# Performance work log

Measured on AMD Instinct MI355X. Metric: run time of the kernel, lower is better.

The kernel has to match this reference:

```python
import jax, jax.numpy as jnp
import numpy as np

N_EMB = 1024
N_HEAD = 16
HD = N_EMB // N_HEAD
ROPE_BASE = 10000.0


def _rope_cos_sin(seq_len, dim, dtype):
    inv_freq = 1.0 / (ROPE_BASE ** (jnp.arange(0, dim, 2, dtype=jnp.float32) / dim))
    t = jnp.arange(seq_len, dtype=jnp.float32)
    freqs = jnp.outer(t, inv_freq)              # [S, dim/2]
    emb = jnp.concatenate([freqs, freqs], -1)    # [S, dim]
    return jnp.cos(emb).astype(dtype), jnp.sin(emb).astype(dtype)


def _rotate_half(x):
    x1, x2 = jnp.split(x, 2, axis=-1)
    return jnp.concatenate([-x2, x1], axis=-1)


def _apply_rope(x):
    # x: [B, H, L, hd]; rotary over sequence axis (-2)
    cos, sin = _rope_cos_sin(x.shape[-2], x.shape[-1], x.dtype)
    return x * cos + _rotate_half(x) * sin


def setup_inputs() -> dict:
    key = jax.random.key(0)
    ks = jax.random.split(key, 8)
    B, T, S = 2, 2048, 2048
    std = 0.02
    return {
        "x": jax.random.normal(ks[0], (B, T, N_EMB), jnp.float32),
        "memory": jax.random.normal(ks[1], (B, S, N_EMB), jnp.float32),
        "q_w": jax.random.normal(ks[2], (N_EMB, N_EMB), jnp.float32) * std,
        "q_b": jnp.zeros((N_EMB,), jnp.float32),
        "kv_w": jax.random.normal(ks[3], (N_EMB, 2 * N_EMB), jnp.float32) * std,
        "kv_b": jnp.zeros((2 * N_EMB,), jnp.float32),
        "proj_w": jax.random.normal(ks[4], (N_EMB, N_EMB), jnp.float32) * std,
        "proj_b": jnp.zeros((N_EMB,), jnp.float32),
    }


def reference(x, memory, q_w, q_b, kv_w, kv_b, proj_w, proj_b):
    B, S, C = memory.shape
    T = x.shape[1]
    kv = memory @ kv_w + kv_b                      # [B,S,2C]
    K, V = jnp.split(kv, 2, axis=-1)
    Q = x @ q_w + q_b                              # [B,T,C]

    def heads(t, L):
        return t.reshape(B, L, N_HEAD, HD).transpose(0, 2, 1, 3)

    Q, K, V = heads(Q, T), heads(K, S), heads(V, S)
    Q = jax.nn.elu(Q) + 1.0                        # positive feature map
    K = jax.nn.elu(K) + 1.0
    Q_rot = _apply_rope(Q)
    K_rot = _apply_rope(K)
    # denom row-sum: sum_s Q.K_s == Q . (sum_s K_s) -- identical math, no SxT matrix
    denom = jnp.einsum('bhtd,bhd->bht', Q, K.sum(axis=2))[..., None]  # [B,H,T,1]
    att = jnp.einsum('bhtd,bhsd->bhts', Q_rot, K_rot) / denom          # [B,H,T,S]
    y = jnp.einsum('bhts,bhsd->bhtd', att, V)                          # [B,H,T,hd]
    y = y.transpose(0, 2, 1, 3).reshape(B, T, C)
    return y @ proj_w + proj_b
```

## Files before the change

### kernel.cpp

```cpp
#include <hip/hip_runtime.h>
#include <cstddef>
#include <cstdint>

#define B_SZ  2
#define T_SEQ 2048
#define S_SEQ 2048
#define C_EMB 1024
#define NH    16
#define HD    64
#define KDIM  1024

typedef __attribute__((ext_vector_type(8))) short bf16x8;
typedef __attribute__((ext_vector_type(4))) float f32x4;

#define OFF_XH    ((size_t)0)
#define OFF_XL    ((size_t)2097152)
#define OFF_MEMH  ((size_t)4194304)
#define OFF_MEML  ((size_t)6291456)
#define OFF_QWH   ((size_t)8388608)
#define OFF_QWL   ((size_t)8912896)
#define OFF_KVWH  ((size_t)9437184)
#define OFF_KVWL  ((size_t)10485760)
#define OFF_PWH   ((size_t)11534336)
#define OFF_PWL   ((size_t)12058624)
#define OFF_KSUM  ((size_t)12582912)
#define OFF_MT    ((size_t)12584960)
#define OFF_TAB   ((size_t)12716032)
#define OFF_YH    ((size_t)12847104)
#define OFF_YL    ((size_t)14944256)
#define WS_FLOATS ((size_t)17041408)

__device__ __forceinline__ float elu1(float v) {
    return v > 0.0f ? v + 1.0f : __expf(v);
}
__device__ __forceinline__ unsigned short bf16_rne(float x) {
    union { float f; unsigned int u; } v; v.f = x;
    unsigned int u = v.u;
    return (unsigned short)((u + 0x7FFFu + ((u >> 16) & 1u)) >> 16);
}
__device__ __forceinline__ float bf16_to_f(unsigned short h) {
    union { unsigned int u; float f; } v; v.u = ((unsigned int)h) << 16;
    return v.f;
}

#define PREP_BLOCKS 13064

__device__ __forceinline__ void split4_body(
    const float4* __restrict__ in, ushort4* __restrict__ hi,
    ushort4* __restrict__ lo, int i)
{
    float4 v = in[i];
    ushort4 h, l;
    h.x = bf16_rne(v.x); l.x = bf16_rne(v.x - bf16_to_f(h.x));
    h.y = bf16_rne(v.y); l.y = bf16_rne(v.y - bf16_to_f(h.y));
    h.z = bf16_rne(v.z); l.z = bf16_rne(v.z - bf16_to_f(h.z));
    h.w = bf16_rne(v.w); l.w = bf16_rne(v.w - bf16_to_f(h.w));
    hi[i] = h; lo[i] = l;
}

__device__ __forceinline__ void transpose_body(
    const float* __restrict__ W, unsigned short* __restrict__ Wth,
    unsigned short* __restrict__ Wtl, int K, int N, int bx, int by,
    float (*tile)[33])
{
    const int k0 = by * 32, n0 = bx * 32;
    const int tx = threadIdx.x & 31, ty = threadIdx.x >> 5;
    #pragma unroll
    for (int j = 0; j < 4; ++j)
        tile[ty + j * 8][tx] = W[(size_t)(k0 + ty + j * 8) * N + n0 + tx];
    __syncthreads();
    #pragma unroll
    for (int j = 0; j < 4; ++j) {
        float x = tile[tx][ty + j * 8];
        unsigned short h = bf16_rne(x);
        unsigned short l = bf16_rne(x - bf16_to_f(h));
        size_t o = (size_t)(n0 + ty + j * 8) * K + k0 + tx;
        Wth[o] = h; Wtl[o] = l;
    }
}

__global__ __launch_bounds__(256) void prep_kernel(
    const float* __restrict__ x, const float* __restrict__ memory,
    const float* __restrict__ q_w, const float* __restrict__ kv_w,
    const float* __restrict__ proj_w,
    unsigned short* __restrict__ xh, unsigned short* __restrict__ xl,
    unsigned short* __restrict__ mh, unsigned short* __restrict__ ml,
    unsigned short* __restrict__ qwh, unsigned short* __restrict__ qwl,
    unsigned short* __restrict__ kvwh, unsigned short* __restrict__ kvwl,
    unsigned short* __restrict__ pwh, unsigned short* __restrict__ pwl,
    float2* __restrict__ tab, float* __restrict__ zero_base)
{
    __shared__ float tile[32][33];
    const int bid = blockIdx.x;
    const int tid = threadIdx.x;
    if (bid < 4096) {
        split4_body((const float4*)x, (ushort4*)xh, (ushort4*)xl, bid * 256 + tid);
    } else if (bid < 8192) {
        split4_body((const float4*)memory, (ushort4*)mh, (ushort4*)ml, (bid - 4096) * 256 + tid);
    } else if (bid < 9216) {
        int i = bid - 8192;
        transpose_body(q_w, qwh, qwl, 1024, 1024, i & 31, i >> 5, tile);
    } else if (bid < 11264) {
        int i = bid - 9216;
        transpose_body(kv_w, kvwh, kvwl, 1024, 2048, i & 63, i >> 6, tile);
    } else if (bid < 12288) {
        int i = bid - 11264;
        transpose_body(proj_w, pwh, pwl, 1024, 1024, i & 31, i >> 5, tile);
    } else if (bid < 12544) {
        int idx = (bid - 12288) * 256 + tid;
        int pos = idx >> 5, i = idx & 31;
        double invf = exp(-(double)i * (9.210340371976184 / 32.0));
        float arg = (float)((double)pos * invf);
        float sn, cs;
        sincosf(arg, &sn, &cs);
        tab[idx] = make_float2(cs, sn);
    } else {
        int idx = (bid - 12544) * 256 + tid;
        if (idx < 2048 + 131072) zero_base[idx] = 0.0f;
    }
}

#define WAITCNT_VM(N)   asm volatile("s_waitcnt vmcnt(" #N ")" ::: "memory")
#define WAITCNT_LGKM(N) asm volatile("s_waitcnt lgkmcnt(" #N ")" ::: "memory")
#define CBAR()          asm volatile("" ::: "memory")

template<int BN, int M_IT, bool KV>
__device__ __forceinline__ void gemm_pipe(
    const unsigned short* __restrict__ Ah, const unsigned short* __restrict__ Al,
    const unsigned short* __restrict__ Bth, const unsigned short* __restrict__ Btl,
    unsigned short* lds, int m0, int n0, f32x4 (&acc)[M_IT][4])
{
    constexpr int BUFSZ = 16384 + 2 * BN * 32;
    constexpr int NT = KDIM / 32;
    const int tid = threadIdx.x;
    const int w = tid >> 6, lane = tid & 63;
    const int quad = lane >> 4, lrow = lane & 15;
    const int sr = tid >> 2;
    const int g  = (tid & 3) ^ ((tid >> 3) & 3);
    constexpr int WAVES_N = (BN == 128) ? 2 : 1;
    const int wr = (WAVES_N == 2) ? (w >> 1) : w;
    const int wc = (WAVES_N == 2) ? (w & 1) : 0;
    const int rowbase = wr * (M_IT * 16);
    const int colbase = wc * 64;
    const int sw = ((quad ^ ((lrow >> 1) & 3)) << 3);

    const unsigned short* gA0 = Ah + (size_t)(m0 + sr) * KDIM + g * 8;
    const unsigned short* gA1 = Ah + (size_t)(m0 + 128 + sr) * KDIM + g * 8;
    const unsigned short* gA2 = Al + (size_t)(m0 + sr) * KDIM + g * 8;
    const unsigned short* gA3 = Al + (size_t)(m0 + 128 + sr) * KDIM + g * 8;
    const unsigned short* gB0;
    const unsigned short* gB1 = nullptr;
    if constexpr (KV) {
        size_t brow = (size_t)(n0 + sr) + (sr >= 64 ? (size_t)960 : 0);
        gB0 = Bth + brow * KDIM + g * 8;
        gB1 = Btl + brow * KDIM + g * 8;
    } else {
        const unsigned short* bsrc = (w < 4) ? Bth : Btl;
        gB0 = bsrc + (size_t)(n0 + (sr & 63)) * KDIM + g * 8;
    }
    const int lA0 = w * 512;
    const int lA1 = 4096 + w * 512;
    const int lA2 = 8192 + w * 512;
    const int lA3 = 12288 + w * 512;
    int lB0, lB1 = 0;
    if constexpr (KV) {
        lB0 = 16384 + w * 512;
        lB1 = 20480 + w * 512;
    } else {
        lB0 = 16384 + ((w >= 4) ? 2048 : 0) + (w & 3) * 512;
    }

    auto STAGE = [&](unsigned short* buf, int k0) {
        __builtin_amdgcn_global_load_lds(
            (const __attribute__((address_space(1))) unsigned int*)(gA0 + k0),
            (__attribute__((address_space(3))) unsigned int*)(buf + lA0), 16, 0, 0);
        __builtin_amdgcn_global_load_lds(
            (const __attribute__((address_space(1))) unsigned int*)(gA1 + k0),
            (__attribute__((address_space(3))) unsigned int*)(buf + lA1), 16, 0, 0);
        __builtin_amdgcn_global_load_lds(
            (const __attribute__((address_space(1))) unsigned int*)(gA2 + k0),
            (__attribute__((address_space(3))) unsigned int*)(buf + lA2), 16, 0, 0);
        __builtin_amdgcn_global_load_lds(
            (const __attribute__((address_space(1))) unsigned int*)(gA3 + k0),
            (__attribute__((address_space(3))) unsigned int*)(buf + lA3), 16, 0, 0);
        __builtin_amdgcn_global_load_lds(
            (const __attribute__((address_space(1))) unsigned int*)(gB0 + k0),
            (__attribute__((address_space(3))) unsigned int*)(buf + lB0), 16, 0, 0);
        if constexpr (KV)
            __builtin_amdgcn_global_load_lds(
                (const __attribute__((address_space(1))) unsigned int*)(gB1 + k0),
                (__attribute__((address_space(3))) unsigned int*)(buf + lB1), 16, 0, 0);
    };

    unsigned short* cur = lds;
    unsigned short* nxt = lds + BUFSZ;
    unsigned short* thr = lds + 2 * BUFSZ;
    STAGE(cur, 0);
    STAGE(nxt, 32);

    #pragma unroll 1
    for (int t = 0; t < NT; ++t) {
        if (t == NT - 1) {
            WAITCNT_VM(0);
        } else {
            if constexpr (KV) { WAITCNT_VM(6); } else { WAITCNT_VM(5); }
        }
        __builtin_amdgcn_s_barrier();

        bf16x8 ah[M_IT], al[M_IT], bh[4], bl[4];
        #pragma unroll
        for (int it = 0; it < M_IT; ++it) {
            int off = (rowbase + it * 16 + lrow) * 32 + sw;
            ah[it] = *(const bf16x8*)&cur[off];
            al[it] = *(const bf16x8*)&cur[8192 + off];
        }
        #pragma unroll
        for (int jt = 0; jt < 2; ++jt) {
            int boff = (colbase + jt * 16 + lrow) * 32 + sw;
            bh[jt] = *(const bf16x8*)&cur[16384 + boff];
            bl[jt] = *(const bf16x8*)&cur[16384 + BN * 32 + boff];
        }
        CBAR();
        #pragma unroll
        for (int jt = 2; jt < 4; ++jt) {
            int boff = (colbase + jt * 16 + lrow) * 32 + sw;
            bh[jt] = *(const bf16x8*)&cur[16384 + boff];
            bl[jt] = *(const bf16x8*)&cur[16384 + BN * 32 + boff];
        }
        if (t + 2 < NT) STAGE(thr, (t + 2) * 32);

        WAITCNT_LGKM(4);
        __builtin_amdgcn_sched_barrier(0);
        __builtin_amdgcn_s_setprio(1);
        #pragma unroll
        for (int it = 0; it < M_IT; ++it)
            #pragma unroll
            for (int jt = 0; jt < 2; ++jt)
                acc[it][jt] = __builtin_amdgcn_mfma_f32_16x16x32_bf16(ah[it], bh[jt], acc[it][jt], 0, 0, 0);
        #pragma unroll
        for (int it = 0; it < M_IT; ++it)
            #pragma unroll
            for (int jt = 0; jt < 2; ++jt)
                acc[it][jt] = __builtin_amdgcn_mfma_f32_16x16x32_bf16(ah[it], bl[jt], acc[it][jt], 0, 0, 0);
        #pragma unroll
        for (int it = 0; it < M_IT; ++it)
            #pragma unroll
            for (int jt = 0; jt < 2; ++jt)
                acc[it][jt] = __builtin_amdgcn_mfma_f32_16x16x32_bf16(al[it], bh[jt], acc[it][jt], 0, 0, 0);

        WAITCNT_LGKM(0);
        __builtin_amdgcn_sched_barrier(0);
        #pragma unroll
        for (int it = 0; it < M_IT; ++it)
            #pragma unroll
            for (int jt = 2; jt < 4; ++jt)
                acc[it][jt] = __builtin_amdgcn_mfma_f32_16x16x32_bf16(ah[it], bh[jt], acc[it][jt], 0, 0, 0);
        #pragma unroll
        for (int it = 0; it < M_IT; ++it)
            #pragma unroll
            for (int jt = 2; jt < 4; ++jt)
                acc[it][jt] = __builtin_amdgcn_mfma_f32_16x16x32_bf16(ah[it], bl[jt], acc[it][jt], 0, 0, 0);
        #pragma unroll
        for (int it = 0; it < M_IT; ++it)
            #pragma unroll
            for (int jt = 2; jt < 4; ++jt)
                acc[it][jt] = __builtin_amdgcn_mfma_f32_16x16x32_bf16(al[it], bh[jt], acc[it][jt], 0, 0, 0);
        __builtin_amdgcn_s_setprio(0);

        unsigned short* tmp = cur; cur = nxt; nxt = thr; thr = tmp;
    }
    __syncthreads();
}

__device__ __forceinline__ void xcd_swz16(int& bx, int& by) {
    int id = (int)(blockIdx.x + (blockIdx.y << 4));
    int x = id & 7, k = id >> 3;
    bx = k >> 1;
    by = x * 2 + (k & 1);
}

__global__ __launch_bounds__(512) void gemm_kv(
    const unsigned short* __restrict__ Ah, const unsigned short* __restrict__ Al,
    const unsigned short* __restrict__ Bth, const unsigned short* __restrict__ Btl,
    const float* __restrict__ bias, const float2* __restrict__ tab,
    float* __restrict__ Ksum, float* __restrict__ Mt)
{
    __shared__ alignas(16) unsigned short smem[73728];
    const int tid = threadIdx.x;
    const int w = tid >> 6, lane = tid & 63;
    const int wr = w >> 1, wc = w & 1;
    const int quad = lane >> 4, lrow = lane & 15;
    int h, mt;
    xcd_swz16(h, mt);
    const int m0 = mt * 256;
    const int b  = m0 >> 11;
    const int tbase = (m0 & 2047) + wr * 64;
    const int bh_idx = b * NH + h;

    f32x4 acc[4][4] = {};
    gemm_pipe<128, 4, true>(Ah, Al, Bth, Btl, smem, m0, h * 64, acc);

    const bool isK = (wc == 0);
    const int colg = (isK ? 0 : C_EMB) + h * 64;
    float bb[4];
    #pragma unroll
    for (int jt = 0; jt < 4; ++jt) bb[jt] = bias[colg + jt * 16 + lrow];
    #pragma unroll
    for (int it = 0; it < 4; ++it)
        #pragma unroll
        for (int jt = 0; jt < 4; ++jt)
            #pragma unroll
            for (int r = 0; r < 4; ++r) {
                float v = acc[it][jt][r] + bb[jt];
                acc[it][jt][r] = isK ? elu1(v) : v;
            }

    if (isK) {
        #pragma unroll
        for (int jt = 0; jt < 4; ++jt) {
            float p = 0.0f;
            #pragma unroll
            for (int it = 0; it < 4; ++it)
                #pragma unroll
                for (int r = 0; r < 4; ++r) p += acc[it][jt][r];
            p += __shfl_xor(p, 16);
            p += __shfl_xor(p, 32);
            if (quad == 0)
                atomicAdd(&Ksum[b * C_EMB + h * 64 + jt * 16 + lrow], p);
        }
        #pragma unroll
        for (int it = 0; it < 4; ++it)
            #pragma unroll
            for (int r = 0; r < 4; ++r) {
                int s = tbase + it * 16 + quad * 4 + r;
                float2 c0 = tab[s * 32 + lrow];
                float2 c1 = tab[s * 32 + 16 + lrow];
                float a0 = acc[it][0][r], a1 = acc[it][1][r];
                float a2 = acc[it][2][r], a3 = acc[it][3][r];
                acc[it][0][r] = a0 * c0.x - a2 * c0.y;
                acc[it][2][r] = a2 * c0.x + a0 * c0.y;
                acc[it][1][r] = a1 * c1.x - a3 * c1.y;
                acc[it][3][r] = a3 * c1.x + a1 * c1.y;
            }
    }

    unsigned short* Hd = smem + (isK ? 0 : 33792);
    unsigned short* Ld = Hd + 16896;
    #pragma unroll
    for (int jt = 0; jt < 4; ++jt) {
        int d = jt * 16 + lrow;
        #pragma unroll
        for (int it = 0; it < 4; ++it) {
            int t0loc = wr * 64 + it * 16 + quad * 4;
            ushort4 h4, l4;
            float v0 = acc[it][jt][0], v1 = acc[it][jt][1];
            float v2 = acc[it][jt][2], v3 = acc[it][jt][3];
            h4.x = bf16_rne(v0); l4.x = bf16_rne(v0 - bf16_to_f(h4.x));
            h4.y = bf16_rne(v1); l4.y = bf16_rne(v1 - bf16_to_f(h4.y));
            h4.z = bf16_rne(v2); l4.z = bf16_rne(v2 - bf16_to_f(h4.z));
            h4.w = bf16_rne(v3); l4.w = bf16_rne(v3 - bf16_to_f(h4.w));
            *(ushort4*)&Hd[d * 264 + t0loc] = h4;
            *(ushort4*)&Ld[d * 264 + t0loc] = l4;
        }
    }
    __syncthreads();

    {
        const unsigned short* KH = smem;
        const unsigned short* KL = smem + 16896;
        const unsigned short* VH = smem + 33792;
        const unsigned short* VL = smem + 50688;
        const int mrow = (w & 3) * 16 + lrow;
        const int thalf = w >> 2;
        f32x4 macc[4] = {};
        #pragma unroll
        for (int ks = 0; ks < 4; ++ks) {
            int kof = thalf * 128 + ks * 32 + quad * 8;
            bf16x8 vah = *(const bf16x8*)&VH[mrow * 264 + kof];
            bf16x8 val = *(const bf16x8*)&VL[mrow * 264 + kof];
            #pragma unroll
            for (int jt = 0; jt < 4; ++jt) {
                int nrow = jt * 16 + lrow;
                bf16x8 kbh = *(const bf16x8*)&KH[nrow * 264 + kof];
                bf16x8 kbl = *(const bf16x8*)&KL[nrow * 264 + kof];
                macc[jt] = __builtin_amdgcn_mfma_f32_16x16x32_bf16(vah, kbh, macc[jt], 0, 0, 0);
                macc[jt] = __builtin_amdgcn_mfma_f32_16x16x32_bf16(vah, kbl, macc[jt], 0, 0, 0);
                macc[jt] = __builtin_amdgcn_mfma_f32_16x16x32_bf16(val, kbh, macc[jt], 0, 0, 0);
            }
        }
        #pragma unroll
        for (int jt = 0; jt < 4; ++jt)
            #pragma unroll
            for (int r = 0; r < 4; ++r)
                atomicAdd(&Mt[((size_t)bh_idx * 64 + (w & 3) * 16 + quad * 4 + r) * 64 + jt * 16 + lrow],
                          macc[jt][r]);
    }
}

__global__ __launch_bounds__(512) void gemm_q(
    const unsigned short* __restrict__ Ah, const unsigned short* __restrict__ Al,
    const unsigned short* __restrict__ Bth, const unsigned short* __restrict__ Btl,
    const float* __restrict__ bias, const float2* __restrict__ tab,
    const float* __restrict__ Ksum, const float* __restrict__ Mt,
    unsigned short* __restrict__ Yh, unsigned short* __restrict__ Yl)
{
    __shared__ alignas(16) unsigned short smem[61440];
    int h, mt;
    xcd_swz16(h, mt);
    const int m0 = mt * 256;
    f32x4 acc[2][4] = {};
    gemm_pipe<64, 2, false>(Ah, Al, Bth, Btl, smem, m0, h * 64, acc);

    const int tid = threadIdx.x;
    const int w = tid >> 6, lane = tid & 63;
    const int quad = lane >> 4, lrow = lane & 15;
    const int b = m0 >> 11;
    const int tbase = (m0 & 2047) + w * 32;
    const int bh = b * NH + h;

    float bb[4];
    #pragma unroll
    for (int jt = 0; jt < 4; ++jt) bb[jt] = bias[h * 64 + jt * 16 + lrow];
    #pragma unroll
    for (int it = 0; it < 2; ++it)
        #pragma unroll
        for (int jt = 0; jt < 4; ++jt)
            #pragma unroll
            for (int r = 0; r < 4; ++r)
                acc[it][jt][r] = elu1(acc[it][jt][r] + bb[jt]);

    float ks[4], den_reg[2][4];
    #pragma unroll
    for (int jt = 0; jt < 4; ++jt) ks[jt] = Ksum[b * C_EMB + h * 64 + jt * 16 + lrow];
    #pragma unroll
    for (int it = 0; it < 2; ++it)
        #pragma unroll
        for (int r = 0; r < 4; ++r) {
            float p = acc[it][0][r] * ks[0] + acc[it][1][r] * ks[1]
                    + acc[it][2][r] * ks[2] + acc[it][3][r] * ks[3];
            p += __shfl_xor(p, 1);
            p += __shfl_xor(p, 2);
            p += __shfl_xor(p, 4);
            p += __shfl_xor(p, 8);
            den_reg[it][r] = p;
        }

    #pragma unroll
    for (int it = 0; it < 2; ++it)
        #pragma unroll
        for (int r = 0; r < 4; ++r) {
            int s = tbase + it * 16 + quad * 4 + r;
            float2 c0 = tab[s * 32 + lrow];
            float2 c1 = tab[s * 32 + 16 + lrow];
            float a0 = acc[it][0][r], a1 = acc[it][1][r];
            float a2 = acc[it][2][r], a3 = acc[it][3][r];
            acc[it][0][r] = a0 * c0.x - a2 * c0.y;
            acc[it][2][r] = a2 * c0.x + a0 * c0.y;
            acc[it][1][r] = a1 * c1.x - a3 * c1.y;
            acc[it][3][r] = a3 * c1.x + a1 * c1.y;
        }

    unsigned short* QH = smem + w * 4608;
    unsigned short* QL = QH + 2304;
    #pragma unroll
    for (int it = 0; it < 2; ++it)
        #pragma unroll
        for (int jt = 0; jt < 4; ++jt)
            #pragma unroll
            for (int r = 0; r < 4; ++r) {
                int tloc = it * 16 + quad * 4 + r;
                int d = jt * 16 + lrow;
                float v = acc[it][jt][r];
                unsigned short hh = bf16_rne(v);
                QH[tloc * 72 + d] = hh;
                QL[tloc * 72 + d] = bf16_rne(v - bf16_to_f(hh));
            }

    f32x4 acc2[2][4] = {};
    #pragma unroll
    for (int kc = 0; kc < 2; ++kc) {
        bf16x8 mbh[4], mbl[4];
        #pragma unroll
        for (int jt2 = 0; jt2 < 4; ++jt2) {
            const float* mp = &Mt[((size_t)bh * 64 + jt2 * 16 + lrow) * 64 + kc * 32 + quad * 8];
            #pragma unroll
            for (int e = 0; e < 8; ++e) {
                float x = mp[e];
                unsigned short hh = bf16_rne(x);
                mbh[jt2][e] = (short)hh;
                mbl[jt2][e] = (short)bf16_rne(x - bf16_to_f(hh));
            }
        }
        #pragma unroll
        for (int it2 = 0; it2 < 2; ++it2) {
            int ro = (it2 * 16 + lrow) * 72 + kc * 32 + quad * 8;
            bf16x8 qh = *(const bf16x8*)&QH[ro];
            bf16x8 ql = *(const bf16x8*)&QL[ro];
            #pragma unroll
            for (int jt2 = 0; jt2 < 4; ++jt2) {
                acc2[it2][jt2] = __builtin_amdgcn_mfma_f32_16x16x32_bf16(qh, mbh[jt2], acc2[it2][jt2], 0, 0, 0);
                acc2[it2][jt2] = __builtin_amdgcn_mfma_f32_16x16x32_bf16(qh, mbl[jt2], acc2[it2][jt2], 0, 0, 0);
                acc2[it2][jt2] = __builtin_amdgcn_mfma_f32_16x16x32_bf16(ql, mbh[jt2], acc2[it2][jt2], 0, 0, 0);
            }
        }
    }

    #pragma unroll
    for (int it2 = 0; it2 < 2; ++it2)
        #pragma unroll
        for (int jt2 = 0; jt2 < 4; ++jt2)
            #pragma unroll
            for (int r = 0; r < 4; ++r) {
                float v = acc2[it2][jt2][r] / den_reg[it2][r];
                size_t o = ((size_t)(m0 + w * 32 + it2 * 16 + quad * 4 + r)) * C_EMB
                         + h * 64 + jt2 * 16 + lrow;
                unsigned short hh = bf16_rne(v);
                Yh[o] = hh;
                Yl[o] = bf16_rne(v - bf16_to_f(hh));
            }
}

__global__ __launch_bounds__(512) void gemm_out(
    const unsigned short* __restrict__ Ah, const unsigned short* __restrict__ Al,
    const unsigned short* __restrict__ Bth, const unsigned short* __restrict__ Btl,
    const float* __restrict__ bias, float* __restrict__ out)
{
    __shared__ alignas(16) unsigned short smem[61440];
    int nt, mt;
    xcd_swz16(nt, mt);
    const int m0 = mt * 256, n0 = nt * 64;
    f32x4 acc[2][4] = {};
    gemm_pipe<64, 2, false>(Ah, Al, Bth, Btl, smem, m0, n0, acc);

    const int tid = threadIdx.x;
    const int w = tid >> 6, lane = tid & 63;
    const int quad = lane >> 4, lrow = lane & 15;

    #pragma unroll
    for (int jt = 0; jt < 4; ++jt) {
        int gc = n0 + jt * 16 + lrow;
        float bb = bias[gc];
        #pragma unroll
        for (int it = 0; it < 2; ++it) {
            int grb = m0 + w * 32 + it * 16 + quad * 4;
            #pragma unroll
            for (int r = 0; r < 4; ++r)
                out[(size_t)(grb + r) * C_EMB + gc] = acc[it][jt][r] + bb;
        }
    }
}

extern "C" void kernel_launch(void* const* d_in, const int* in_sizes, int n_in,
                              void* d_out, int out_size, void* d_ws, size_t ws_size,
                              hipStream_t stream)
{
    const float* x      = (const float*)d_in[0];
    const float* memory = (const float*)d_in[1];
    const float* q_w    = (const float*)d_in[2];
    const float* q_b    = (const float*)d_in[3];
    const float* kv_w   = (const float*)d_in[4];
    const float* kv_b   = (const float*)d_in[5];
    const float* proj_w = (const float*)d_in[6];
    const float* proj_b = (const float*)d_in[7];

    if (ws_size < WS_FLOATS * sizeof(float)) return;

    float* ws = (float*)d_ws;
    unsigned short* xh   = (unsigned short*)(ws + OFF_XH);
    unsigned short* xl   = (unsigned short*)(ws + OFF_XL);
    unsigned short* mh   = (unsigned short*)(ws + OFF_MEMH);
    unsigned short* ml   = (unsigned short*)(ws + OFF_MEML);
    unsigned short* qwh  = (unsigned short*)(ws + OFF_QWH);
    unsigned short* qwl  = (unsigned short*)(ws + OFF_QWL);
    unsigned short* kvwh = (unsigned short*)(ws + OFF_KVWH);
    unsigned short* kvwl = (unsigned short*)(ws + OFF_KVWL);
    unsigned short* pwh  = (unsigned short*)(ws + OFF_PWH);
    unsigned short* pwl  = (unsigned short*)(ws + OFF_PWL);
    unsigned short* Yh   = (unsigned short*)(ws + OFF_YH);
    unsigned short* Yl   = (unsigned short*)(ws + OFF_YL);
    float*  Ksum = ws + OFF_KSUM;
    float*  Mm   = ws + OFF_MT;
    float2* tab  = (float2*)(ws + OFF_TAB);

    prep_kernel<<<PREP_BLOCKS, 256, 0, stream>>>(
        x, memory, q_w, kv_w, proj_w,
        xh, xl, mh, ml, qwh, qwl, kvwh, kvwl, pwh, pwl,
        tab, Ksum );

    gemm_kv<<<dim3(16, 16), 512, 0, stream>>>(mh, ml, kvwh, kvwl, kv_b, tab, Ksum, Mm);
    gemm_q<<<dim3(16, 16), 512, 0, stream>>>(xh, xl, qwh, qwl, q_b, tab, Ksum, Mm, Yh, Yl);
    gemm_out<<<dim3(16, 16), 512, 0, stream>>>(Yh, Yl, pwh, pwl, proj_b, (float*)d_out);
}
```

Measured before the change: 222.4 us.

## Restructure GEMM pipelines: register double-buffered KV loop, smaller 128-row Q/out tiles

Replaces the shared triple-buffered gemm_pipe with two specialised loops. gemm_kv now uses two LDS buffers and ping-pongs operand registers, so LDS reads for the next K-step overlap the current MFMAs. It also lowers its LDS footprint and requests two blocks per CU. gemm_q and gemm_out switch to 256-thread blocks with 128-row tiles, double-buffered LDS and a 32-way XCD swizzle, doubling the grid to raise occupancy. The trade-off is fuller waits (vmcnt 0) each step, which can expose load latency, plus smaller tiles with less reuse per block.

```diff
diff --git a/kernel.cpp b/kernel.cpp
--- a/kernel.cpp
+++ b/kernel.cpp
@@ -124,168 +124,26 @@
 #define WAITCNT_LGKM(N) asm volatile("s_waitcnt lgkmcnt(" #N ")" ::: "memory")
 #define CBAR()          asm volatile("" ::: "memory")
 
-template<int BN, int M_IT, bool KV>
-__device__ __forceinline__ void gemm_pipe(
-    const unsigned short* __restrict__ Ah, const unsigned short* __restrict__ Al,
-    const unsigned short* __restrict__ Bth, const unsigned short* __restrict__ Btl,
-    unsigned short* lds, int m0, int n0, f32x4 (&acc)[M_IT][4])
-{
-    constexpr int BUFSZ = 16384 + 2 * BN * 32;
-    constexpr int NT = KDIM / 32;
-    const int tid = threadIdx.x;
-    const int w = tid >> 6, lane = tid & 63;
-    const int quad = lane >> 4, lrow = lane & 15;
-    const int sr = tid >> 2;
-    const int g  = (tid & 3) ^ ((tid >> 3) & 3);
-    constexpr int WAVES_N = (BN == 128) ? 2 : 1;
-    const int wr = (WAVES_N == 2) ? (w >> 1) : w;
-    const int wc = (WAVES_N == 2) ? (w & 1) : 0;
-    const int rowbase = wr * (M_IT * 16);
-    const int colbase = wc * 64;
-    const int sw = ((quad ^ ((lrow >> 1) & 3)) << 3);
-
-    const unsigned short* gA0 = Ah + (size_t)(m0 + sr) * KDIM + g * 8;
-    const unsigned short* gA1 = Ah + (size_t)(m0 + 128 + sr) * KDIM + g * 8;
-    const unsigned short* gA2 = Al + (size_t)(m0 + sr) * KDIM + g * 8;
-    const unsigned short* gA3 = Al + (size_t)(m0 + 128 + sr) * KDIM + g * 8;
-    const unsigned short* gB0;
-    const unsigned short* gB1 = nullptr;
-    if constexpr (KV) {
-        size_t brow = (size_t)(n0 + sr) + (sr >= 64 ? (size_t)960 : 0);
-        gB0 = Bth + brow * KDIM + g * 8;
-        gB1 = Btl + brow * KDIM + g * 8;
-    } else {
-        const unsigned short* bsrc = (w < 4) ? Bth : Btl;
-        gB0 = bsrc + (size_t)(n0 + (sr & 63)) * KDIM + g * 8;
-    }
-    const int lA0 = w * 512;
-    const int lA1 = 4096 + w * 512;
-    const int lA2 = 8192 + w * 512;
-    const int lA3 = 12288 + w * 512;
-    int lB0, lB1 = 0;
-    if constexpr (KV) {
-        lB0 = 16384 + w * 512;
-        lB1 = 20480 + w * 512;
-    } else {
-        lB0 = 16384 + ((w >= 4) ? 2048 : 0) + (w & 3) * 512;
-    }
-
-    auto STAGE = [&](unsigned short* buf, int k0) {
-        __builtin_amdgcn_global_load_lds(
-            (const __attribute__((address_space(1))) unsigned int*)(gA0 + k0),
-            (__attribute__((address_space(3))) unsigned int*)(buf + lA0), 16, 0, 0);
-        __builtin_amdgcn_global_load_lds(
-            (const __attribute__((address_space(1))) unsigned int*)(gA1 + k0),
-            (__attribute__((address_space(3))) unsigned int*)(buf + lA1), 16, 0, 0);
-        __builtin_amdgcn_global_load_lds(
-            (const __attribute__((address_space(1))) unsigned int*)(gA2 + k0),
-            (__attribute__((address_space(3))) unsigned int*)(buf + lA2), 16, 0, 0);
-        __builtin_amdgcn_global_load_lds(
-            (const __attribute__((address_space(1))) unsigned int*)(gA3 + k0),
-            (__attribute__((address_space(3))) unsigned int*)(buf + lA3), 16, 0, 0);
-        __builtin_amdgcn_global_load_lds(
-            (const __attribute__((address_space(1))) unsigned int*)(gB0 + k0),
-            (__attribute__((address_space(3))) unsigned int*)(buf + lB0), 16, 0, 0);
-        if constexpr (KV)
-            __builtin_amdgcn_global_load_lds(
-                (const __attribute__((address_space(1))) unsigned int*)(gB1 + k0),
-                (__attribute__((address_space(3))) unsigned int*)(buf + lB1), 16, 0, 0);
-    };
-
-    unsigned short* cur = lds;
-    unsigned short* nxt = lds + BUFSZ;
-    unsigned short* thr = lds + 2 * BUFSZ;
-    STAGE(cur, 0);
-    STAGE(nxt, 32);
-
-    #pragma unroll 1
-    for (int t = 0; t < NT; ++t) {
-        if (t == NT - 1) {
-            WAITCNT_VM(0);
-        } else {
-            if constexpr (KV) { WAITCNT_VM(6); } else { WAITCNT_VM(5); }
-        }
-        __builtin_amdgcn_s_barrier();
-
-        bf16x8 ah[M_IT], al[M_IT], bh[4], bl[4];
-        #pragma unroll
-        for (int it = 0; it < M_IT; ++it) {
-            int off = (rowbase + it * 16 + lrow) * 32 + sw;
-            ah[it] = *(const bf16x8*)&cur[off];
-            al[it] = *(const bf16x8*)&cur[8192 + off];
-        }
-        #pragma unroll
-        for (int jt = 0; jt < 2; ++jt) {
-            int boff = (colbase + jt * 16 + lrow) * 32 + sw;
-            bh[jt] = *(const bf16x8*)&cur[16384 + boff];
-            bl[jt] = *(const bf16x8*)&cur[16384 + BN * 32 + boff];
-        }
-        CBAR();
-        #pragma unroll
-        for (int jt = 2; jt < 4; ++jt) {
-            int boff = (colbase + jt * 16 + lrow) * 32 + sw;
-            bh[jt] = *(const bf16x8*)&cur[16384 + boff];
-            bl[jt] = *(const bf16x8*)&cur[16384 + BN * 32 + boff];
-        }
-        if (t + 2 < NT) STAGE(thr, (t + 2) * 32);
-
-        WAITCNT_LGKM(4);
-        __builtin_amdgcn_sched_barrier(0);
-        __builtin_amdgcn_s_setprio(1);
-        #pragma unroll
-        for (int it = 0; it < M_IT; ++it)
-            #pragma unroll
-            for (int jt = 0; jt < 2; ++jt)
-                acc[it][jt] = __builtin_amdgcn_mfma_f32_16x16x32_bf16(ah[it], bh[jt], acc[it][jt], 0, 0, 0);
-        #pragma unroll
-        for (int it = 0; it < M_IT; ++it)
-            #pragma unroll
-            for (int jt = 0; jt < 2; ++jt)
-                acc[it][jt] = __builtin_amdgcn_mfma_f32_16x16x32_bf16(ah[it], bl[jt], acc[it][jt], 0, 0, 0);
-        #pragma unroll
-        for (int it = 0; it < M_IT; ++it)
-            #pragma unroll
-            for (int jt = 0; jt < 2; ++jt)
-                acc[it][jt] = __builtin_amdgcn_mfma_f32_16x16x32_bf16(al[it], bh[jt], acc[it][jt], 0, 0, 0);
-
-        WAITCNT_LGKM(0);
-        __builtin_amdgcn_sched_barrier(0);
-        #pragma unroll
-        for (int it = 0; it < M_IT; ++it)
-            #pragma unroll
-            for (int jt = 2; jt < 4; ++jt)
-                acc[it][jt] = __builtin_amdgcn_mfma_f32_16x16x32_bf16(ah[it], bh[jt], acc[it][jt], 0, 0, 0);
-        #pragma unroll
-        for (int it = 0; it < M_IT; ++it)
-            #pragma unroll
-            for (int jt = 2; jt < 4; ++jt)
-                acc[it][jt] = __builtin_amdgcn_mfma_f32_16x16x32_bf16(ah[it], bl[jt], acc[it][jt], 0, 0, 0);
-        #pragma unroll
-        for (int it = 0; it < M_IT; ++it)
-            #pragma unroll
-            for (int jt = 2; jt < 4; ++jt)
-                acc[it][jt] = __builtin_amdgcn_mfma_f32_16x16x32_bf16(al[it], bh[jt], acc[it][jt], 0, 0, 0);
-        __builtin_amdgcn_s_setprio(0);
-
-        unsigned short* tmp = cur; cur = nxt; nxt = thr; thr = tmp;
-    }
-    __syncthreads();
-}
-
 __device__ __forceinline__ void xcd_swz16(int& bx, int& by) {
     int id = (int)(blockIdx.x + (blockIdx.y << 4));
     int x = id & 7, k = id >> 3;
     bx = k >> 1;
     by = x * 2 + (k & 1);
 }
-
-__global__ __launch_bounds__(512) void gemm_kv(
+__device__ __forceinline__ void xcd_swz32(int& bx, int& by) {
+    int id = (int)(blockIdx.x + (blockIdx.y << 4));
+    int x = id & 7, k = id >> 3;
+    bx = k >> 2;
+    by = x * 4 + (k & 3);
+}
+
+__global__ __launch_bounds__(512, 2) void gemm_kv(
     const unsigned short* __restrict__ Ah, const unsigned short* __restrict__ Al,
     const unsigned short* __restrict__ Bth, const unsigned short* __restrict__ Btl,
     const float* __restrict__ bias, const float2* __restrict__ tab,
     float* __restrict__ Ksum, float* __restrict__ Mt)
 {
-    __shared__ alignas(16) unsigned short smem[73728];
+    __shared__ alignas(16) unsigned short smem[67584];
     const int tid = threadIdx.x;
     const int w = tid >> 6, lane = tid & 63;
     const int wr = w >> 1, wc = w & 1;
@@ -293,12 +151,124 @@
     int h, mt;
     xcd_swz16(h, mt);
     const int m0 = mt * 256;
+    const int n0 = h * 64;
     const int b  = m0 >> 11;
     const int tbase = (m0 & 2047) + wr * 64;
     const int bh_idx = b * NH + h;
 
+    const int sr = tid >> 2;
+    const int g  = (tid & 3) ^ ((tid >> 3) & 3);
+    const unsigned short* gA0 = Ah + (size_t)(m0 + sr) * KDIM + g * 8;
+    const unsigned short* gA1 = Ah + (size_t)(m0 + 128 + sr) * KDIM + g * 8;
+    const unsigned short* gA2 = Al + (size_t)(m0 + sr) * KDIM + g * 8;
+    const unsigned short* gA3 = Al + (size_t)(m0 + 128 + sr) * KDIM + g * 8;
+    const size_t brow = (size_t)(n0 + sr) + (sr >= 64 ? (size_t)960 : 0);
+    const unsigned short* gB0 = Bth + brow * KDIM + g * 8;
+    const unsigned short* gB1 = Btl + brow * KDIM + g * 8;
+    const int lA0 = w * 512;
+    const int lA1 = 4096 + w * 512;
+    const int lA2 = 8192 + w * 512;
+    const int lA3 = 12288 + w * 512;
+    const int lB0 = 16384 + w * 512;
+    const int lB1 = 20480 + w * 512;
+
+    auto STAGE = [&](unsigned short* buf, int k0) {
+        __builtin_amdgcn_global_load_lds(
+            (const __attribute__((address_space(1))) unsigned int*)(gA0 + k0),
+            (__attribute__((address_space(3))) unsigned int*)(buf + lA0), 16, 0, 0);
+        __builtin_amdgcn_global_load_lds(
+            (const __attribute__((address_space(1))) unsigned int*)(gA1 + k0),
+            (__attribute__((address_space(3))) unsigned int*)(buf + lA1), 16, 0, 0);
+        __builtin_amdgcn_global_load_lds(
+            (const __attribute__((address_space(1))) unsigned int*)(gA2 + k0),
+            (__attribute__((address_space(3))) unsigned int*)(buf + lA2), 16, 0, 0);
+        __builtin_amdgcn_global_load_lds(
+            (const __attribute__((address_space(1))) unsigned int*)(gA3 + k0),
+            (__attribute__((address_space(3))) unsigned int*)(buf + lA3), 16, 0, 0);
+        __builtin_amdgcn_global_load_lds(
+            (const __attribute__((address_space(1))) unsigned int*)(gB0 + k0),
+            (__attribute__((address_space(3))) unsigned int*)(buf + lB0), 16, 0, 0);
+        __builtin_amdgcn_global_load_lds(
+            (const __attribute__((address_space(1))) unsigned int*)(gB1 + k0),
+            (__attribute__((address_space(3))) unsigned int*)(buf + lB1), 16, 0, 0);
+    };
+
+    const int rowbase = wr * 64, colbase = wc * 64;
+    const int sw = ((quad ^ ((lrow >> 1) & 3)) << 3);
+
     f32x4 acc[4][4] = {};
-    gemm_pipe<128, 4, true>(Ah, Al, Bth, Btl, smem, m0, h * 64, acc);
+    bf16x8 ahA[4], alA[4], bhA[4], blA[4];
+    bf16x8 ahB[4], alB[4], bhB[4], blB[4];
+
+    auto KV_READ = [&](bf16x8 (&AH)[4], bf16x8 (&AL)[4],
+                       bf16x8 (&BH)[4], bf16x8 (&BL)[4],
+                       const unsigned short* _b) {
+        #pragma unroll
+        for (int it = 0; it < 4; ++it) {
+            int off = (rowbase + it * 16 + lrow) * 32 + sw;
+            AH[it] = *(const bf16x8*)&_b[off];
+            AL[it] = *(const bf16x8*)&_b[8192 + off];
+        }
+        #pragma unroll
+        for (int jt = 0; jt < 4; ++jt) {
+            int boff = (colbase + jt * 16 + lrow) * 32 + sw;
+            BH[jt] = *(const bf16x8*)&_b[16384 + boff];
+            BL[jt] = *(const bf16x8*)&_b[20480 + boff];
+        }
+    };
+    auto KV_MFMA = [&](bf16x8 (&AH)[4], bf16x8 (&AL)[4],
+                       bf16x8 (&BH)[4], bf16x8 (&BL)[4]) {
+        #pragma unroll
+        for (int it = 0; it < 4; ++it)
+            #pragma unroll
+            for (int jt = 0; jt < 4; ++jt)
+                acc[it][jt] = __builtin_amdgcn_mfma_f32_16x16x32_bf16(AH[it], BH[jt], acc[it][jt], 0, 0, 0);
+        #pragma unroll
+        for (int it = 0; it < 4; ++it)
+            #pragma unroll
+            for (int jt = 0; jt < 4; ++jt)
+                acc[it][jt] = __builtin_amdgcn_mfma_f32_16x16x32_bf16(AH[it], BL[jt], acc[it][jt], 0, 0, 0);
+        #pragma unroll
+        for (int it = 0; it < 4; ++it)
+            #pragma unroll
+            for (int jt = 0; jt < 4; ++jt)
+                acc[it][jt] = __builtin_amdgcn_mfma_f32_16x16x32_bf16(AL[it], BH[jt], acc[it][jt], 0, 0, 0);
+    };
+
+    unsigned short* buf0 = smem;
+    unsigned short* buf1 = smem + 24576;
+
+    STAGE(buf0, 0);
+    STAGE(buf1, 32);
+    WAITCNT_VM(6);
+    __builtin_amdgcn_s_barrier();
+    KV_READ(ahA, alA, bhA, blA, buf0);
+
+    #pragma unroll 1
+    for (int t = 0; t < 32; t += 2) {
+        WAITCNT_VM(0);
+        WAITCNT_LGKM(0);
+        __builtin_amdgcn_sched_barrier(0);
+        __builtin_amdgcn_s_barrier();
+        __builtin_amdgcn_sched_barrier(0);
+        if (t + 2 < 32) STAGE(buf0, (t + 2) * 32);
+        KV_READ(ahB, alB, bhB, blB, buf1);
+        __builtin_amdgcn_s_setprio(1);
+        KV_MFMA(ahA, alA, bhA, blA);
+        __builtin_amdgcn_s_setprio(0);
+
+        WAITCNT_VM(0);
+        WAITCNT_LGKM(0);
+        __builtin_amdgcn_sched_barrier(0);
+        __builtin_amdgcn_s_barrier();
+        __builtin_amdgcn_sched_barrier(0);
+        if (t + 3 < 32) STAGE(buf1, (t + 3) * 32);
+        if (t + 2 < 32) KV_READ(ahA, alA, bhA, blA, buf0);
+        __builtin_amdgcn_s_setprio(1);
+        KV_MFMA(ahB, alB, bhB, blB);
+        __builtin_amdgcn_s_setprio(0);
+    }
+    __syncthreads();
 
     const bool isK = (wc == 0);
     const int colg = (isK ? 0 : C_EMB) + h * 64;
@@ -397,19 +367,136 @@
     }
 }
 
-__global__ __launch_bounds__(512) void gemm_q(
+__device__ __forceinline__ void gemm_main_128(
+    const unsigned short* __restrict__ Ah, const unsigned short* __restrict__ Al,
+    const unsigned short* __restrict__ Bth, const unsigned short* __restrict__ Btl,
+    unsigned short* lds, int m0, int n0, f32x4 (&acc)[2][4])
+{
+    const int tid = threadIdx.x;
+    const int w = tid >> 6, lane = tid & 63;
+    const int quad = lane >> 4, lrow = lane & 15;
+    const int srow = lane >> 2;
+    const int g  = (lane & 3) ^ ((lane >> 3) & 3);
+    const int sw = ((quad ^ ((lrow >> 1) & 3)) << 3);
+
+    const unsigned short* gA0 = Ah + (size_t)(m0 + w * 16 + srow) * KDIM + g * 8;
+    const unsigned short* gA1 = Ah + (size_t)(m0 + 64 + w * 16 + srow) * KDIM + g * 8;
+    const unsigned short* gA2 = Al + (size_t)(m0 + w * 16 + srow) * KDIM + g * 8;
+    const unsigned short* gA3 = Al + (size_t)(m0 + 64 + w * 16 + srow) * KDIM + g * 8;
+    const unsigned short* gB0 = Bth + (size_t)(n0 + w * 16 + srow) * KDIM + g * 8;
+    const unsigned short* gB1 = Btl + (size_t)(n0 + w * 16 + srow) * KDIM + g * 8;
+    const int lA0 = w * 512, lA1 = 2048 + w * 512;
+    const int lA2 = 4096 + w * 512, lA3 = 6144 + w * 512;
+    const int lB0 = 8192 + w * 512, lB1 = 10240 + w * 512;
+
+    auto STAGE = [&](unsigned short* buf, int k0) {
+        __builtin_amdgcn_global_load_lds(
+            (const __attribute__((address_space(1))) unsigned int*)(gA0 + k0),
+            (__attribute__((address_space(3))) unsigned int*)(buf + lA0), 16, 0, 0);
+        __builtin_amdgcn_global_load_lds(
+            (const __attribute__((address_space(1))) unsigned int*)(gA1 + k0),
+            (__attribute__((address_space(3))) unsigned int*)(buf + lA1), 16, 0, 0);
+        __builtin_amdgcn_global_load_lds(
+            (const __attribute__((address_space(1))) unsigned int*)(gA2 + k0),
+            (__attribute__((address_space(3))) unsigned int*)(buf + lA2), 16, 0, 0);
+        __builtin_amdgcn_global_load_lds(
+            (const __attribute__((address_space(1))) unsigned int*)(gA3 + k0),
+            (__attribute__((address_space(3))) unsigned int*)(buf + lA3), 16, 0, 0);
+        __builtin_amdgcn_global_load_lds(
+            (const __attribute__((address_space(1))) unsigned int*)(gB0 + k0),
+            (__attribute__((address_space(3))) unsigned int*)(buf + lB0), 16, 0, 0);
+        __builtin_amdgcn_global_load_lds(
+            (const __attribute__((address_space(1))) unsigned int*)(gB1 + k0),
+            (__attribute__((address_space(3))) unsigned int*)(buf + lB1), 16, 0, 0);
+    };
+
+    STAGE(lds, 0);
+
+    #pragma unroll 1
+    for (int t = 0; t < 32; ++t) {
+        unsigned short* cur = lds + (t & 1) * 12288;
+        unsigned short* nxt = lds + ((t + 1) & 1) * 12288;
+        WAITCNT_VM(0);
+        __builtin_amdgcn_sched_barrier(0);
+        __builtin_amdgcn_s_barrier();
+        __builtin_amdgcn_sched_barrier(0);
+
+        bf16x8 ah[2], al[2], bh[4], bl[4];
+        #pragma unroll
+        for (int it = 0; it < 2; ++it) {
+            int off = (w * 32 + it * 16 + lrow) * 32 + sw;
+            ah[it] = *(const bf16x8*)&cur[off];
+            al[it] = *(const bf16x8*)&cur[4096 + off];
+        }
+        #pragma unroll
+        for (int jt = 0; jt < 2; ++jt) {
+            int boff = (jt * 16 + lrow) * 32 + sw;
+            bh[jt] = *(const bf16x8*)&cur[8192 + boff];
+            bl[jt] = *(const bf16x8*)&cur[10240 + boff];
+        }
+        CBAR();
+        #pragma unroll
+        for (int jt = 2; jt < 4; ++jt) {
+            int boff = (jt * 16 + lrow) * 32 + sw;
+            bh[jt] = *(const bf16x8*)&cur[8192 + boff];
+            bl[jt] = *(const bf16x8*)&cur[10240 + boff];
+        }
+        if (t + 1 < 32) STAGE(nxt, (t + 1) * 32);
+
+        WAITCNT_LGKM(4);
+        __builtin_amdgcn_sched_barrier(0);
+        __builtin_amdgcn_s_setprio(1);
+        #pragma unroll
+        for (int it = 0; it < 2; ++it)
+            #pragma unroll
+            for (int jt = 0; jt < 2; ++jt)
+                acc[it][jt] = __builtin_amdgcn_mfma_f32_16x16x32_bf16(ah[it], bh[jt], acc[it][jt], 0, 0, 0);
+        #pragma unroll
+        for (int it = 0; it < 2; ++it)
+            #pragma unroll
+            for (int jt = 0; jt < 2; ++jt)
+                acc[it][jt] = __builtin_amdgcn_mfma_f32_16x16x32_bf16(ah[it], bl[jt], acc[it][jt], 0, 0, 0);
+        #pragma unroll
+        for (int it = 0; it < 2; ++it)
+            #pragma unroll
+            for (int jt = 0; jt < 2; ++jt)
+                acc[it][jt] = __builtin_amdgcn_mfma_f32_16x16x32_bf16(al[it], bh[jt], acc[it][jt], 0, 0, 0);
+
+        WAITCNT_LGKM(0);
+        __builtin_amdgcn_sched_barrier(0);
+        #pragma unroll
+        for (int it = 0; it < 2; ++it)
+            #pragma unroll
+            for (int jt = 2; jt < 4; ++jt)
+                acc[it][jt] = __builtin_amdgcn_mfma_f32_16x16x32_bf16(ah[it], bh[jt], acc[it][jt], 0, 0, 0);
+        #pragma unroll
+        for (int it = 0; it < 2; ++it)
+            #pragma unroll
+            for (int jt = 2; jt < 4; ++jt)
+                acc[it][jt] = __builtin_amdgcn_mfma_f32_16x16x32_bf16(ah[it], bl[jt], acc[it][jt], 0, 0, 0);
+        #pragma unroll
+        for (int it = 0; it < 2; ++it)
+            #pragma unroll
+            for (int jt = 2; jt < 4; ++jt)
+                acc[it][jt] = __builtin_amdgcn_mfma_f32_16x16x32_bf16(al[it], bh[jt], acc[it][jt], 0, 0, 0);
+        __builtin_amdgcn_s_setprio(0);
+    }
+    __syncthreads();
+}
+
+__global__ __launch_bounds__(256, 3) void gemm_q(
     const unsigned short* __restrict__ Ah, const unsigned short* __restrict__ Al,
     const unsigned short* __restrict__ Bth, const unsigned short* __restrict__ Btl,
     const float* __restrict__ bias, const float2* __restrict__ tab,
     const float* __restrict__ Ksum, const float* __restrict__ Mt,
     unsigned short* __restrict__ Yh, unsigned short* __restrict__ Yl)
 {
-    __shared__ alignas(16) unsigned short smem[61440];
+    __shared__ alignas(16) unsigned short smem[24576];
     int h, mt;
-    xcd_swz16(h, mt);
-    const int m0 = mt * 256;
+    xcd_swz32(h, mt);
+    const int m0 = mt * 128;
     f32x4 acc[2][4] = {};
-    gemm_pipe<64, 2, false>(Ah, Al, Bth, Btl, smem, m0, h * 64, acc);
+    gemm_main_128(Ah, Al, Bth, Btl, smem, m0, h * 64, acc);
 
     const int tid = threadIdx.x;
     const int w = tid >> 6, lane = tid & 63;
@@ -520,17 +607,17 @@
             }
 }
 
-__global__ __launch_bounds__(512) void gemm_out(
+__global__ __launch_bounds__(256, 3) void gemm_out(
     const unsigned short* __restrict__ Ah, const unsigned short* __restrict__ Al,
     const unsigned short* __restrict__ Bth, const unsigned short* __restrict__ Btl,
     const float* __restrict__ bias, float* __restrict__ out)
 {
-    __shared__ alignas(16) unsigned short smem[61440];
+    __shared__ alignas(16) unsigned short smem[24576];
     int nt, mt;
-    xcd_swz16(nt, mt);
-    const int m0 = mt * 256, n0 = nt * 64;
+    xcd_swz32(nt, mt);
+    const int m0 = mt * 128, n0 = nt * 64;
     f32x4 acc[2][4] = {};
-    gemm_pipe<64, 2, false>(Ah, Al, Bth, Btl, smem, m0, n0, acc);
+    gemm_main_128(Ah, Al, Bth, Btl, smem, m0, n0, acc);
 
     const int tid = threadIdx.x;
     const int w = tid >> 6, lane = tid & 63;
@@ -588,6 +675,6 @@
         tab, Ksum );
 
     gemm_kv<<<dim3(16, 16), 512, 0, stream>>>(mh, ml, kvwh, kvwl, kv_b, tab, Ksum, Mm);
-    gemm_q<<<dim3(16, 16), 512, 0, stream>>>(xh, xl, qwh, qwl, q_b, tab, Ksum, Mm, Yh, Yl);
-    gemm_out<<<dim3(16, 16), 512, 0, stream>>>(Yh, Yl, pwh, pwl, proj_b, (float*)d_out);
-}
+    gemm_q<<<dim3(16, 32), 256, 0, stream>>>(xh, xl, qwh, qwl, q_b, tab, Ksum, Mm, Yh, Yl);
+    gemm_out<<<dim3(16, 32), 256, 0, stream>>>(Yh, Yl, pwh, pwl, proj_b, (float*)d_out);
+}
```

New measurement: 242.9 us. 1.09x slower.
